# Kernel tuning notes

Measured on AMD Instinct MI355X. Metric: run time of the kernel, lower is better.

## Reference

```python
import jax, jax.numpy as jnp
import numpy as np

NUM_EXPERTS = 8


def setup_inputs() -> dict:
    key = jax.random.key(0)
    k1, k2, k3, k4, k5 = jax.random.split(key, 5)
    T, D, DFF, E, K = 2048, 2048, 1024, NUM_EXPERTS, 2
    hidden_states = jax.random.normal(k1, (T, D), dtype=jnp.float32)
    w1 = jax.random.normal(k2, (E, 2 * DFF, D), dtype=jnp.float32) * 0.02
    w2 = jax.random.normal(k3, (E, D, DFF), dtype=jnp.float32) * 0.02
    topk_weights = jax.random.uniform(k4, (T, K), dtype=jnp.float32)
    topk_weights = topk_weights / jnp.sum(topk_weights, axis=-1, keepdims=True)
    topk_ids = jax.random.randint(k5, (T, K), 0, E, dtype=jnp.int32)
    return {"hidden_states": hidden_states, "w1": w1, "w2": w2,
            "topk_weights": topk_weights, "topk_ids": topk_ids}


def _expert_fn(x, w1_e, w2_e):
    # x: [T, D], w1_e: [2*DFF, D], w2_e: [D, DFF]
    gu = x @ w1_e.T                      # [T, 2*DFF]
    dff = w2_e.shape[1]
    gate, up = gu[:, :dff], gu[:, dff:]
    h = jax.nn.silu(gate) * up           # SiLU-and-mul activation
    return h @ w2_e.T                    # [T, D]


def reference(hidden_states, w1, w2, topk_weights, topk_ids):
    T = hidden_states.shape[0]
    E = w1.shape[0]
    # route[t, e] = sum_k topk_weights[t,k] * (topk_ids[t,k] == e)
    route = jnp.zeros((T, E), dtype=hidden_states.dtype)
    route = route.at[jnp.arange(T)[:, None], topk_ids].add(topk_weights)
    # per-expert dense GEMMs (E is small and fixed), then weighted combine
    outs = jax.vmap(lambda w1_e, w2_e: _expert_fn(hidden_states, w1_e, w2_e))(w1, w2)  # [E, T, D]
    return jnp.einsum('te,etd->td', route, outs)
```

## Files before the change

### kernel.cpp

```cpp
#include <hip/hip_runtime.h>
#include <hip/hip_bf16.h>
#include <stdint.h>

typedef __attribute__((ext_vector_type(4))) float f32x4;
typedef __attribute__((ext_vector_type(8))) short bf16x8;
typedef unsigned short u16;

#define T_TOK   2048
#define D_DIM   2048
#define DFF_DIM 1024
#define NEXP    8
#define TOPK    2
#define NROWS   (T_TOK * TOPK)
#define BM      128
#define BK      64
#define MAX_MB  40
#define NBLK1   16
#define NBLK2   16
#define GRID_G  (NBLK1 * MAX_MB)

__device__ __forceinline__ u16 f2bf(float f) {
    __hip_bfloat16 h = __float2bfloat16(f);
    return *reinterpret_cast<u16*>(&h);
}

__device__ __forceinline__ void gll16(const u16* gsrc, const u16* lds) {
    __builtin_amdgcn_global_load_lds(
        (const __attribute__((address_space(1))) uint32_t*)gsrc,
        (__attribute__((address_space(3))) uint32_t*)lds, 16, 0, 0);
}

__device__ __forceinline__ bf16x8 lds_read8_swz(const u16* base, int row, int inner) {
    int off = row * 128 + (inner ^ ((row & 7) << 4));
    return *(const bf16x8*)((const char*)base + off);
}

__global__ void cvt_x_kernel(const float* __restrict__ X, u16* __restrict__ Xb) {
    int idx = (blockIdx.x * 256 + threadIdx.x) * 8;
    f32x4 a = *(const f32x4*)(X + idx);
    f32x4 b = *(const f32x4*)(X + idx + 4);
    bf16x8 v;
#pragma unroll
    for (int j = 0; j < 4; ++j) { v[j] = (short)f2bf(a[j]); v[j + 4] = (short)f2bf(b[j]); }
    *(bf16x8*)(Xb + idx) = v;
}

__global__ void route_kernel(const int* __restrict__ topk_ids,
                             const float* __restrict__ topk_w,
                             int* __restrict__ sched,
                             int* __restrict__ row_token,
                             float* __restrict__ row_w) {
    __shared__ int cnt[NEXP], off[NEXP], cur[NEXP];
    const int tid = threadIdx.x;
    if (tid < NEXP) cnt[tid] = 0;
    __syncthreads();
    for (int p = tid; p < NROWS; p += blockDim.x)
        atomicAdd(&cnt[topk_ids[p]], 1);
    __syncthreads();
    if (tid == 0) {
        int acc = 0, mb = 0;
        for (int e = 0; e < NEXP; ++e) {
            off[e] = acc;
            int c = cnt[e];
            for (int m0 = 0; m0 < c; m0 += BM) {
                sched[1 + 3 * mb] = e;
                sched[2 + 3 * mb] = acc + m0;
                sched[3 + 3 * mb] = (c - m0 < BM) ? (c - m0) : BM;
                ++mb;
            }
            acc += c;
        }
        sched[0] = mb;
    }
    if (tid < NEXP) cur[tid] = 0;
    __syncthreads();
    for (int p = tid; p < NROWS; p += blockDim.x) {
        int e = topk_ids[p];
        int slot = off[e] + atomicAdd(&cur[e], 1);
        row_token[slot] = p / TOPK;
        row_w[slot]     = topk_w[p];
    }
}

__global__ __launch_bounds__(256, 3)
void gemm1_kernel(const u16* __restrict__ Xb, const float* __restrict__ w1,
                  const int* __restrict__ sched, const int* __restrict__ row_token,
                  u16* __restrict__ H) {
    __shared__ u16 lA[2][BM * BK];
    __shared__ u16 lB[BM * BK];

    const int bid = blockIdx.x;
    const int swz = (bid & 7) * (GRID_G / 8) + (bid >> 3);
    const int mb  = swz >> 4;
    if (mb >= sched[0]) return;
    const int e    = sched[1 + 3 * mb];
    const int m0   = sched[2 + 3 * mb];
    const int mlen = sched[3 + 3 * mb];
    const int n0   = (swz & 15) * 64;

    const int tid  = threadIdx.x;
    const int lane = tid & 63;
    const int wave = tid >> 6;
    const int wm = wave >> 1, wn = wave & 1;
    const int lr = lane & 15, lk = lane >> 4;

    const u16* asrc[4];
    int aoff[4];
#pragma unroll
    for (int i = 0; i < 4; ++i) {
        int R = i * 32 + wave * 8 + (lane >> 3);
        int grow = m0 + R; if (grow > NROWS - 1) grow = NROWS - 1;
        int tok = row_token[grow];
        asrc[i] = Xb + (size_t)tok * D_DIM + (size_t)(((lane & 7) ^ (R & 7)) * 8);
        aoff[i] = i * 2048 + wave * 512;
    }
    const float* bptr[4];
    int wroff[4];
#pragma unroll
    for (int i = 0; i < 4; ++i) {
        int chunk = i * 256 + tid;
        int row = chunk >> 3, c8 = chunk & 7;
        int gcol = (row < 64) ? (n0 + row) : (DFF_DIM + n0 + (row - 64));
        bptr[i] = w1 + ((size_t)e * (2 * DFF_DIM) + gcol) * D_DIM + c8 * 8;
        wroff[i] = row * 128 + ((c8 * 16) ^ ((row & 7) << 4));
    }

    f32x4 rb[4][2];
    f32x4 accg[4][2], accu[4][2];
#pragma unroll
    for (int m = 0; m < 4; ++m)
#pragma unroll
        for (int n = 0; n < 2; ++n) {
            accg[m][n] = (f32x4){0.f, 0.f, 0.f, 0.f};
            accu[m][n] = (f32x4){0.f, 0.f, 0.f, 0.f};
        }

#pragma unroll
    for (int i = 0; i < 4; ++i) gll16(asrc[i], &lA[0][aoff[i]]);
#pragma unroll
    for (int i = 0; i < 4; ++i) {
        rb[i][0] = *(const f32x4*)(bptr[i]);
        rb[i][1] = *(const f32x4*)(bptr[i] + 4);
    }
#pragma unroll
    for (int i = 0; i < 4; ++i) {
        bf16x8 vb;
#pragma unroll
        for (int j = 0; j < 4; ++j) { vb[j] = (short)f2bf(rb[i][0][j]); vb[j + 4] = (short)f2bf(rb[i][1][j]); }
        *(bf16x8*)((char*)lB + wroff[i]) = vb;
    }
    __syncthreads();

    int cur = 0;
    const int KT = D_DIM / BK;
    for (int kt = 0; kt < KT; ++kt) {
        if (kt + 1 < KT) {
            int k0 = (kt + 1) * BK;
#pragma unroll
            for (int i = 0; i < 4; ++i) gll16(asrc[i] + k0, &lA[cur ^ 1][aoff[i]]);
#pragma unroll
            for (int i = 0; i < 4; ++i) {
                rb[i][0] = *(const f32x4*)(bptr[i] + k0);
                rb[i][1] = *(const f32x4*)(bptr[i] + k0 + 4);
            }
        }
        asm volatile("" ::: "memory");
#pragma unroll
        for (int ks = 0; ks < 2; ++ks) {
            const int inner = ks * 64 + lk * 16;
            bf16x8 af[4], bg[2], bu[2];
#pragma unroll
            for (int m = 0; m < 4; ++m)
                af[m] = lds_read8_swz(lA[cur], wm * 64 + m * 16 + lr, inner);
#pragma unroll
            for (int n = 0; n < 2; ++n) {
                bg[n] = lds_read8_swz(lB, wn * 32 + n * 16 + lr, inner);
                bu[n] = lds_read8_swz(lB, 64 + wn * 32 + n * 16 + lr, inner);
            }
#pragma unroll
            for (int m = 0; m < 4; ++m)
#pragma unroll
                for (int n = 0; n < 2; ++n) {
                    accg[m][n] = __builtin_amdgcn_mfma_f32_16x16x32_bf16(af[m], bg[n], accg[m][n], 0, 0, 0);
                    accu[m][n] = __builtin_amdgcn_mfma_f32_16x16x32_bf16(af[m], bu[n], accu[m][n], 0, 0, 0);
                }
        }
        __syncthreads();
        if (kt + 1 < KT) {
#pragma unroll
            for (int i = 0; i < 4; ++i) {
                bf16x8 vb;
#pragma unroll
                for (int j = 0; j < 4; ++j) { vb[j] = (short)f2bf(rb[i][0][j]); vb[j + 4] = (short)f2bf(rb[i][1][j]); }
                *(bf16x8*)((char*)lB + wroff[i]) = vb;
            }
        }
        __syncthreads();
        cur ^= 1;
    }

#pragma unroll
    for (int m = 0; m < 4; ++m)
#pragma unroll
        for (int n = 0; n < 2; ++n)
#pragma unroll
            for (int r = 0; r < 4; ++r) {
                int rloc = wm * 64 + m * 16 + (lane >> 4) * 4 + r;
                if (rloc < mlen) {
                    int col = wn * 32 + n * 16 + lr;
                    float g = accg[m][n][r], u = accu[m][n][r];
                    float h = (g / (1.f + __expf(-g))) * u;
                    H[(size_t)(m0 + rloc) * DFF_DIM + n0 + col] = f2bf(h);
                }
            }
}

__global__ __launch_bounds__(256, 3)
void gemm2_kernel(const u16* __restrict__ H, const float* __restrict__ w2,
                  const int* __restrict__ sched, const int* __restrict__ row_token,
                  const float* __restrict__ row_w, float* __restrict__ out) {
    __shared__ u16 lA[2][BM * BK];
    __shared__ u16 lB[BM * BK];

    const int bid = blockIdx.x;
    const int swz = (bid & 7) * (GRID_G / 8) + (bid >> 3);
    const int mb  = swz >> 4;
    if (mb >= sched[0]) return;
    const int e    = sched[1 + 3 * mb];
    const int m0   = sched[2 + 3 * mb];
    const int mlen = sched[3 + 3 * mb];
    const int n0   = (swz & 15) * 128;

    const int tid  = threadIdx.x;
    const int lane = tid & 63;
    const int wave = tid >> 6;
    const int wm = wave >> 1, wn = wave & 1;
    const int lr = lane & 15, lk = lane >> 4;

    const u16* asrc[4];
    int aoff[4];
#pragma unroll
    for (int i = 0; i < 4; ++i) {
        int R = i * 32 + wave * 8 + (lane >> 3);
        int grow = m0 + R; if (grow > NROWS - 1) grow = NROWS - 1;
        asrc[i] = H + (size_t)grow * DFF_DIM + (size_t)(((lane & 7) ^ (R & 7)) * 8);
        aoff[i] = i * 2048 + wave * 512;
    }
    const float* bptr[4];
    int wroff[4];
#pragma unroll
    for (int i = 0; i < 4; ++i) {
        int chunk = i * 256 + tid;
        int row = chunk >> 3, c8 = chunk & 7;
        bptr[i] = w2 + ((size_t)e * D_DIM + (n0 + row)) * DFF_DIM + c8 * 8;
        wroff[i] = row * 128 + ((c8 * 16) ^ ((row & 7) << 4));
    }

    f32x4 rb[4][2];
    f32x4 acc[4][4];
#pragma unroll
    for (int m = 0; m < 4; ++m)
#pragma unroll
        for (int n = 0; n < 4; ++n) acc[m][n] = (f32x4){0.f, 0.f, 0.f, 0.f};

#pragma unroll
    for (int i = 0; i < 4; ++i) gll16(asrc[i], &lA[0][aoff[i]]);
#pragma unroll
    for (int i = 0; i < 4; ++i) {
        rb[i][0] = *(const f32x4*)(bptr[i]);
        rb[i][1] = *(const f32x4*)(bptr[i] + 4);
    }
#pragma unroll
    for (int i = 0; i < 4; ++i) {
        bf16x8 vb;
#pragma unroll
        for (int j = 0; j < 4; ++j) { vb[j] = (short)f2bf(rb[i][0][j]); vb[j + 4] = (short)f2bf(rb[i][1][j]); }
        *(bf16x8*)((char*)lB + wroff[i]) = vb;
    }
    __syncthreads();

    int cur = 0;
    const int KT = DFF_DIM / BK;
    for (int kt = 0; kt < KT; ++kt) {
        if (kt + 1 < KT) {
            int k0 = (kt + 1) * BK;
#pragma unroll
            for (int i = 0; i < 4; ++i) gll16(asrc[i] + k0, &lA[cur ^ 1][aoff[i]]);
#pragma unroll
            for (int i = 0; i < 4; ++i) {
                rb[i][0] = *(const f32x4*)(bptr[i] + k0);
                rb[i][1] = *(const f32x4*)(bptr[i] + k0 + 4);
            }
        }
        asm volatile("" ::: "memory");
#pragma unroll
        for (int ks = 0; ks < 2; ++ks) {
            const int inner = ks * 64 + lk * 16;
            bf16x8 af[4], bfr[4];
#pragma unroll
            for (int m = 0; m < 4; ++m)
                af[m] = lds_read8_swz(lA[cur], wm * 64 + m * 16 + lr, inner);
#pragma unroll
            for (int n = 0; n < 4; ++n)
                bfr[n] = lds_read8_swz(lB, wn * 64 + n * 16 + lr, inner);
#pragma unroll
            for (int m = 0; m < 4; ++m)
#pragma unroll
                for (int n = 0; n < 4; ++n)
                    acc[m][n] = __builtin_amdgcn_mfma_f32_16x16x32_bf16(af[m], bfr[n], acc[m][n], 0, 0, 0);
        }
        __syncthreads();
        if (kt + 1 < KT) {
#pragma unroll
            for (int i = 0; i < 4; ++i) {
                bf16x8 vb;
#pragma unroll
                for (int j = 0; j < 4; ++j) { vb[j] = (short)f2bf(rb[i][0][j]); vb[j + 4] = (short)f2bf(rb[i][1][j]); }
                *(bf16x8*)((char*)lB + wroff[i]) = vb;
            }
        }
        __syncthreads();
        cur ^= 1;
    }

#pragma unroll
    for (int m = 0; m < 4; ++m)
#pragma unroll
        for (int n = 0; n < 4; ++n)
#pragma unroll
            for (int r = 0; r < 4; ++r) {
                int rloc = wm * 64 + m * 16 + (lane >> 4) * 4 + r;
                if (rloc < mlen) {
                    int grow = m0 + rloc;
                    int tok  = row_token[grow];
                    float w  = row_w[grow];
                    int col  = wn * 64 + n * 16 + lr;
                    atomicAdd(&out[(size_t)tok * D_DIM + n0 + col], acc[m][n][r] * w);
                }
            }
}

extern "C" void kernel_launch(void* const* d_in, const int* in_sizes, int n_in,
                              void* d_out, int out_size, void* d_ws, size_t ws_size,
                              hipStream_t stream) {
    const float* X  = (const float*)d_in[0];
    const float* w1 = (const float*)d_in[1];
    const float* w2 = (const float*)d_in[2];
    const float* tw = (const float*)d_in[3];
    const int*   ti = (const int*)d_in[4];

    int*   sched     = (int*)d_ws;
    int*   row_token = (int*)((char*)d_ws + 512);
    float* row_w     = (float*)((char*)d_ws + 512 + 4 * NROWS);
    u16*   Xb        = (u16*)((char*)d_ws + 65536);
    u16*   H         = (u16*)((char*)d_ws + 65536 + (size_t)T_TOK * D_DIM * 2);

    route_kernel<<<1, 256, 0, stream>>>(ti, tw, sched, row_token, row_w);
    cvt_x_kernel<<<(T_TOK * D_DIM) / (256 * 8), 256, 0, stream>>>(X, Xb);
    hipMemsetAsync(d_out, 0, (size_t)out_size * sizeof(float), stream);
    gemm1_kernel<<<GRID_G, 256, 0, stream>>>(Xb, w1, sched, row_token, H);
    gemm2_kernel<<<GRID_G, 256, 0, stream>>>(H, w2, sched, row_token, row_w, (float*)d_out);
}
```

Before: 160.6 us.

## Double-buffer B tiles with two-deep register prefetch and single barrier per step

```diff
diff --git a/kernel.cpp b/kernel.cpp
--- a/kernel.cpp
+++ b/kernel.cpp
@@ -15,9 +15,14 @@
 #define BM      128
 #define BK      64
 #define MAX_MB  40
-#define NBLK1   16
-#define NBLK2   16
-#define GRID_G  (NBLK1 * MAX_MB)
+#define GRID_G  (16 * MAX_MB)
+
+#define PIN() asm volatile("" ::: "memory")
+#define WAITBAR()                                                         \
+    asm volatile("s_waitcnt vmcnt(8) lgkmcnt(0)" ::: "memory");           \
+    __builtin_amdgcn_sched_barrier(0);                                    \
+    __builtin_amdgcn_s_barrier();                                         \
+    __builtin_amdgcn_sched_barrier(0)
 
 __device__ __forceinline__ u16 f2bf(float f) {
     __hip_bfloat16 h = __float2bfloat16(f);
@@ -35,7 +40,28 @@
     return *(const bf16x8*)((const char*)base + off);
 }
 
-__global__ void cvt_x_kernel(const float* __restrict__ X, u16* __restrict__ Xb) {
+#define GLL_A(k0, dst)                                                    \
+    _Pragma("unroll") for (int i = 0; i < 4; ++i)                         \
+        gll16(asrc[i] + (k0), &(dst)[aoff[i]]);
+
+#define LOAD_RB(rb, k0)                                                   \
+    _Pragma("unroll") for (int i = 0; i < 4; ++i) {                       \
+        rb[i][0] = *(const f32x4*)(bptr[i] + (k0));                       \
+        rb[i][1] = *(const f32x4*)(bptr[i] + (k0) + 4);                   \
+    }
+
+#define CVT_WRITE(rb, dst)                                                \
+    _Pragma("unroll") for (int i = 0; i < 4; ++i) {                       \
+        bf16x8 vb;                                                        \
+        _Pragma("unroll") for (int j = 0; j < 4; ++j) {                   \
+            vb[j] = (short)f2bf(rb[i][0][j]);                             \
+            vb[j + 4] = (short)f2bf(rb[i][1][j]);                         \
+        }                                                                 \
+        *(bf16x8*)((char*)(dst) + wroff[i]) = vb;                         \
+    }
+
+__global__ void cvt_x_kernel(const float* __restrict__ X, u16* __restrict__ Xb,
+                             float* __restrict__ out) {
     int idx = (blockIdx.x * 256 + threadIdx.x) * 8;
     f32x4 a = *(const f32x4*)(X + idx);
     f32x4 b = *(const f32x4*)(X + idx + 4);
@@ -43,6 +69,9 @@
 #pragma unroll
     for (int j = 0; j < 4; ++j) { v[j] = (short)f2bf(a[j]); v[j + 4] = (short)f2bf(b[j]); }
     *(bf16x8*)(Xb + idx) = v;
+    f32x4 z = (f32x4){0.f, 0.f, 0.f, 0.f};
+    *(f32x4*)(out + idx) = z;
+    *(f32x4*)(out + idx + 4) = z;
 }
 
 __global__ void route_kernel(const int* __restrict__ topk_ids,
@@ -82,12 +111,12 @@
     }
 }
 
-__global__ __launch_bounds__(256, 3)
+__global__ __launch_bounds__(256, 2)
 void gemm1_kernel(const u16* __restrict__ Xb, const float* __restrict__ w1,
                   const int* __restrict__ sched, const int* __restrict__ row_token,
                   u16* __restrict__ H) {
     __shared__ u16 lA[2][BM * BK];
-    __shared__ u16 lB[BM * BK];
+    __shared__ u16 lB[2][BM * BK];
 
     const int bid = blockIdx.x;
     const int swz = (bid & 7) * (GRID_G / 8) + (bid >> 3);
@@ -125,7 +154,7 @@
         wroff[i] = row * 128 + ((c8 * 16) ^ ((row & 7) << 4));
     }
 
-    f32x4 rb[4][2];
+    f32x4 rbA[4][2], rbB[4][2];
     f32x4 accg[4][2], accu[4][2];
 #pragma unroll
     for (int m = 0; m < 4; ++m)
@@ -135,69 +164,57 @@
             accu[m][n] = (f32x4){0.f, 0.f, 0.f, 0.f};
         }
 
-#pragma unroll
-    for (int i = 0; i < 4; ++i) gll16(asrc[i], &lA[0][aoff[i]]);
-#pragma unroll
-    for (int i = 0; i < 4; ++i) {
-        rb[i][0] = *(const f32x4*)(bptr[i]);
-        rb[i][1] = *(const f32x4*)(bptr[i] + 4);
-    }
-#pragma unroll
-    for (int i = 0; i < 4; ++i) {
-        bf16x8 vb;
-#pragma unroll
-        for (int j = 0; j < 4; ++j) { vb[j] = (short)f2bf(rb[i][0][j]); vb[j + 4] = (short)f2bf(rb[i][1][j]); }
-        *(bf16x8*)((char*)lB + wroff[i]) = vb;
-    }
-    __syncthreads();
-
-    int cur = 0;
+#define MFMA_G1(bufA, bufB)                                               \
+    __builtin_amdgcn_s_setprio(1);                                        \
+    _Pragma("unroll") for (int ks = 0; ks < 2; ++ks) {                    \
+        const int inner = ks * 64 + lk * 16;                              \
+        bf16x8 af[4], bg[2], bu[2];                                       \
+        _Pragma("unroll") for (int m = 0; m < 4; ++m)                     \
+            af[m] = lds_read8_swz(bufA, wm * 64 + m * 16 + lr, inner);    \
+        _Pragma("unroll") for (int n = 0; n < 2; ++n) {                   \
+            bg[n] = lds_read8_swz(bufB, wn * 32 + n * 16 + lr, inner);    \
+            bu[n] = lds_read8_swz(bufB, 64 + wn * 32 + n * 16 + lr, inner); \
+        }                                                                 \
+        _Pragma("unroll") for (int m = 0; m < 4; ++m)                     \
+            _Pragma("unroll") for (int n = 0; n < 2; ++n) {               \
+                accg[m][n] = __builtin_amdgcn_mfma_f32_16x16x32_bf16(af[m], bg[n], accg[m][n], 0, 0, 0); \
+                accu[m][n] = __builtin_amdgcn_mfma_f32_16x16x32_bf16(af[m], bu[n], accu[m][n], 0, 0, 0); \
+            }                                                             \
+    }                                                                     \
+    __builtin_amdgcn_s_setprio(0);
+
     const int KT = D_DIM / BK;
-    for (int kt = 0; kt < KT; ++kt) {
-        if (kt + 1 < KT) {
-            int k0 = (kt + 1) * BK;
-#pragma unroll
-            for (int i = 0; i < 4; ++i) gll16(asrc[i] + k0, &lA[cur ^ 1][aoff[i]]);
-#pragma unroll
-            for (int i = 0; i < 4; ++i) {
-                rb[i][0] = *(const f32x4*)(bptr[i] + k0);
-                rb[i][1] = *(const f32x4*)(bptr[i] + k0 + 4);
-            }
-        }
-        asm volatile("" ::: "memory");
-#pragma unroll
-        for (int ks = 0; ks < 2; ++ks) {
-            const int inner = ks * 64 + lk * 16;
-            bf16x8 af[4], bg[2], bu[2];
-#pragma unroll
-            for (int m = 0; m < 4; ++m)
-                af[m] = lds_read8_swz(lA[cur], wm * 64 + m * 16 + lr, inner);
-#pragma unroll
-            for (int n = 0; n < 2; ++n) {
-                bg[n] = lds_read8_swz(lB, wn * 32 + n * 16 + lr, inner);
-                bu[n] = lds_read8_swz(lB, 64 + wn * 32 + n * 16 + lr, inner);
-            }
-#pragma unroll
-            for (int m = 0; m < 4; ++m)
-#pragma unroll
-                for (int n = 0; n < 2; ++n) {
-                    accg[m][n] = __builtin_amdgcn_mfma_f32_16x16x32_bf16(af[m], bg[n], accg[m][n], 0, 0, 0);
-                    accu[m][n] = __builtin_amdgcn_mfma_f32_16x16x32_bf16(af[m], bu[n], accu[m][n], 0, 0, 0);
-                }
-        }
-        __syncthreads();
-        if (kt + 1 < KT) {
-#pragma unroll
-            for (int i = 0; i < 4; ++i) {
-                bf16x8 vb;
-#pragma unroll
-                for (int j = 0; j < 4; ++j) { vb[j] = (short)f2bf(rb[i][0][j]); vb[j + 4] = (short)f2bf(rb[i][1][j]); }
-                *(bf16x8*)((char*)lB + wroff[i]) = vb;
-            }
-        }
-        __syncthreads();
-        cur ^= 1;
-    }
+    GLL_A(0, lA[0]); PIN();
+    LOAD_RB(rbA, 0); PIN();
+    LOAD_RB(rbB, BK); PIN();
+    CVT_WRITE(rbA, lB[0]);
+    WAITBAR();
+
+    for (int tt = 0; tt < KT; tt += 2) {
+        {
+            GLL_A((tt + 1) * BK, lA[1]); PIN();
+            const int kr = (tt + 2 < KT ? tt + 2 : KT - 1) * BK;
+            LOAD_RB(rbA, kr); PIN();
+            MFMA_G1(lA[0], lB[0]);
+            __builtin_amdgcn_sched_barrier(0);
+            CVT_WRITE(rbB, lB[1]);
+            WAITBAR();
+        }
+        {
+            const int t = tt + 1;
+            const int kg = (t + 1 < KT ? t + 1 : KT - 1) * BK;
+            GLL_A(kg, lA[0]); PIN();
+            const int kr = (t + 2 < KT ? t + 2 : KT - 1) * BK;
+            LOAD_RB(rbB, kr); PIN();
+            MFMA_G1(lA[1], lB[1]);
+            if (t + 1 < KT) {
+                __builtin_amdgcn_sched_barrier(0);
+                CVT_WRITE(rbA, lB[0]);
+                WAITBAR();
+            }
+        }
+    }
+#undef MFMA_G1
 
 #pragma unroll
     for (int m = 0; m < 4; ++m)
@@ -215,12 +232,12 @@
             }
 }
 
-__global__ __launch_bounds__(256, 3)
+__global__ __launch_bounds__(256, 2)
 void gemm2_kernel(const u16* __restrict__ H, const float* __restrict__ w2,
                   const int* __restrict__ sched, const int* __restrict__ row_token,
                   const float* __restrict__ row_w, float* __restrict__ out) {
     __shared__ u16 lA[2][BM * BK];
-    __shared__ u16 lB[BM * BK];
+    __shared__ u16 lB[2][BM * BK];
 
     const int bid = blockIdx.x;
     const int swz = (bid & 7) * (GRID_G / 8) + (bid >> 3);
@@ -256,72 +273,60 @@
         wroff[i] = row * 128 + ((c8 * 16) ^ ((row & 7) << 4));
     }
 
-    f32x4 rb[4][2];
+    f32x4 rbA[4][2], rbB[4][2];
     f32x4 acc[4][4];
 #pragma unroll
     for (int m = 0; m < 4; ++m)
 #pragma unroll
         for (int n = 0; n < 4; ++n) acc[m][n] = (f32x4){0.f, 0.f, 0.f, 0.f};
 
-#pragma unroll
-    for (int i = 0; i < 4; ++i) gll16(asrc[i], &lA[0][aoff[i]]);
-#pragma unroll
-    for (int i = 0; i < 4; ++i) {
-        rb[i][0] = *(const f32x4*)(bptr[i]);
-        rb[i][1] = *(const f32x4*)(bptr[i] + 4);
-    }
-#pragma unroll
-    for (int i = 0; i < 4; ++i) {
-        bf16x8 vb;
-#pragma unroll
-        for (int j = 0; j < 4; ++j) { vb[j] = (short)f2bf(rb[i][0][j]); vb[j + 4] = (short)f2bf(rb[i][1][j]); }
-        *(bf16x8*)((char*)lB + wroff[i]) = vb;
-    }
-    __syncthreads();
-
-    int cur = 0;
+#define MFMA_G2(bufA, bufB)                                               \
+    __builtin_amdgcn_s_setprio(1);                                        \
+    _Pragma("unroll") for (int ks = 0; ks < 2; ++ks) {                    \
+        const int inner = ks * 64 + lk * 16;                              \
+        bf16x8 af[4], bfr[4];                                             \
+        _Pragma("unroll") for (int m = 0; m < 4; ++m)                     \
+            af[m] = lds_read8_swz(bufA, wm * 64 + m * 16 + lr, inner);    \
+        _Pragma("unroll") for (int n = 0; n < 4; ++n)                     \
+            bfr[n] = lds_read8_swz(bufB, wn * 64 + n * 16 + lr, inner);   \
+        _Pragma("unroll") for (int m = 0; m < 4; ++m)                     \
+            _Pragma("unroll") for (int n = 0; n < 4; ++n)                 \
+                acc[m][n] = __builtin_amdgcn_mfma_f32_16x16x32_bf16(af[m], bfr[n], acc[m][n], 0, 0, 0); \
+    }                                                                     \
+    __builtin_amdgcn_s_setprio(0);
+
     const int KT = DFF_DIM / BK;
-    for (int kt = 0; kt < KT; ++kt) {
-        if (kt + 1 < KT) {
-            int k0 = (kt + 1) * BK;
-#pragma unroll
-            for (int i = 0; i < 4; ++i) gll16(asrc[i] + k0, &lA[cur ^ 1][aoff[i]]);
-#pragma unroll
-            for (int i = 0; i < 4; ++i) {
-                rb[i][0] = *(const f32x4*)(bptr[i] + k0);
-                rb[i][1] = *(const f32x4*)(bptr[i] + k0 + 4);
-            }
-        }
-        asm volatile("" ::: "memory");
-#pragma unroll
-        for (int ks = 0; ks < 2; ++ks) {
-            const int inner = ks * 64 + lk * 16;
-            bf16x8 af[4], bfr[4];
-#pragma unroll
-            for (int m = 0; m < 4; ++m)
-                af[m] = lds_read8_swz(lA[cur], wm * 64 + m * 16 + lr, inner);
-#pragma unroll
-            for (int n = 0; n < 4; ++n)
-                bfr[n] = lds_read8_swz(lB, wn * 64 + n * 16 + lr, inner);
-#pragma unroll
-            for (int m = 0; m < 4; ++m)
-#pragma unroll
-                for (int n = 0; n < 4; ++n)
-                    acc[m][n] = __builtin_amdgcn_mfma_f32_16x16x32_bf16(af[m], bfr[n], acc[m][n], 0, 0, 0);
-        }
-        __syncthreads();
-        if (kt + 1 < KT) {
-#pragma unroll
-            for (int i = 0; i < 4; ++i) {
-                bf16x8 vb;
-#pragma unroll
-                for (int j = 0; j < 4; ++j) { vb[j] = (short)f2bf(rb[i][0][j]); vb[j + 4] = (short)f2bf(rb[i][1][j]); }
-                *(bf16x8*)((char*)lB + wroff[i]) = vb;
-            }
-        }
-        __syncthreads();
-        cur ^= 1;
-    }
+    GLL_A(0, lA[0]); PIN();
+    LOAD_RB(rbA, 0); PIN();
+    LOAD_RB(rbB, BK); PIN();
+    CVT_WRITE(rbA, lB[0]);
+    WAITBAR();
+
+    for (int tt = 0; tt < KT; tt += 2) {
+        {
+            GLL_A((tt + 1) * BK, lA[1]); PIN();
+            const int kr = (tt + 2 < KT ? tt + 2 : KT - 1) * BK;
+            LOAD_RB(rbA, kr); PIN();
+            MFMA_G2(lA[0], lB[0]);
+            __builtin_amdgcn_sched_barrier(0);
+            CVT_WRITE(rbB, lB[1]);
+            WAITBAR();
+        }
+        {
+            const int t = tt + 1;
+            const int kg = (t + 1 < KT ? t + 1 : KT - 1) * BK;
+            GLL_A(kg, lA[0]); PIN();
+            const int kr = (t + 2 < KT ? t + 2 : KT - 1) * BK;
+            LOAD_RB(rbB, kr); PIN();
+            MFMA_G2(lA[1], lB[1]);
+            if (t + 1 < KT) {
+                __builtin_amdgcn_sched_barrier(0);
+                CVT_WRITE(rbA, lB[0]);
+                WAITBAR();
+            }
+        }
+    }
+#undef MFMA_G2
 
 #pragma unroll
     for (int m = 0; m < 4; ++m)
@@ -356,8 +361,7 @@
     u16*   H         = (u16*)((char*)d_ws + 65536 + (size_t)T_TOK * D_DIM * 2);
 
     route_kernel<<<1, 256, 0, stream>>>(ti, tw, sched, row_token, row_w);
-    cvt_x_kernel<<<(T_TOK * D_DIM) / (256 * 8), 256, 0, stream>>>(X, Xb);
-    hipMemsetAsync(d_out, 0, (size_t)out_size * sizeof(float), stream);
+    cvt_x_kernel<<<(T_TOK * D_DIM) / (256 * 8), 256, 0, stream>>>(X, Xb, (float*)d_out);
     gemm1_kernel<<<GRID_G, 256, 0, stream>>>(Xb, w1, sched, row_token, H);
     gemm2_kernel<<<GRID_G, 256, 0, stream>>>(H, w2, sched, row_token, row_w, (float*)d_out);
 }
```

Result: slower. 219.2 us (+36.4%).
